# Optimization experiments

Measured on AMD Instinct MI355X. Metric: run time of the kernel, lower is better.

## Reference

```python
import jax, jax.numpy as jnp
import numpy as np

B, S, H, NH, DK, VOCAB, FF, L = 512, 64, 512, 8, 64, 2000, 2048, 6


def _pos_enc():
    pos = jnp.arange(S, dtype=jnp.float32)[:, None]           # [S,1]
    i = jnp.arange(H // 2, dtype=jnp.float32)                  # [H/2]
    ang = pos / (10000.0 ** (2.0 * i / H))                     # [S,H/2]
    pe = jnp.zeros((S, H), jnp.float32)
    pe = pe.at[:, 0::2].set(jnp.sin(ang)).at[:, 1::2].set(jnp.cos(ang))
    return pe


def _ln(x, g, b, eps=1e-5):
    m = x.mean(-1, keepdims=True)
    v = ((x - m) ** 2).mean(-1, keepdims=True)
    return (x - m) / jnp.sqrt(v + eps) * g + b


def _heads(x, w):  # x:[B,S,H] w:[H,H] -> [B,NH,S,DK]
    return (x @ w.T).reshape(B, S, NH, DK).transpose(0, 2, 1, 3)


def _sdpa(Q, K, V, keep):  # keep: bool mask broadcastable to [B,NH,S,S]
    scores = jnp.einsum('bhqd,bhkd->bhqk', Q, K) / np.sqrt(DK).astype(np.float32)
    scores = jnp.where(keep, scores, -1e9)
    return jnp.einsum('bhqk,bhkd->bhqd', jax.nn.softmax(scores, axis=-1), V)


def _merge(z, wo):  # [B,NH,S,DK] -> [B,S,H] -> out proj
    return z.transpose(0, 2, 1, 3).reshape(B, S, H) @ wo.T


def setup_inputs():
    key = jax.random.key(0)
    ks = jax.random.split(key, 30)
    n = lambda k, sh: jax.random.normal(k, sh, jnp.float32) * 0.02
    inp = {
        'source_ids': jax.random.randint(ks[0], (B, S), 0, VOCAB),
        'target_ids': jax.random.randint(ks[1], (B, S), 0, VOCAB),
        'source_mask': jnp.ones((B, S), jnp.int32),
        'target_mask': jnp.ones((B, S), jnp.int32),
        'src_emb': n(ks[2], (VOCAB, H)),
        'tgt_emb': n(ks[3], (VOCAB, H)),
        'enc_wq': n(ks[4], (L, H, H)), 'enc_wk': n(ks[5], (L, H, H)),
        'enc_wv': n(ks[6], (L, H, H)), 'enc_wo': n(ks[7], (L, H, H)),
        'enc_ln_g': jnp.ones((L, H), jnp.float32), 'enc_ln_b': jnp.zeros((L, H), jnp.float32),
        'enc_fc1_w': n(ks[8], (L, FF, H)), 'enc_fc1_b': jnp.zeros((L, FF), jnp.float32),
        'enc_fc2_w': n(ks[9], (L, H, FF)), 'enc_fc2_b': jnp.zeros((L, H), jnp.float32),
        'dec_mwq': n(ks[10], (L, H, H)), 'dec_mwk': n(ks[11], (L, H, H)),
        'dec_mwv': n(ks[12], (L, H, H)), 'dec_mwo': n(ks[13], (L, H, H)),
        'dec_cwq': n(ks[14], (L, H, H)), 'dec_cwo': n(ks[15], (L, H, H)),
        'dec_ln_g': jnp.ones((L, H), jnp.float32), 'dec_ln_b': jnp.zeros((L, H), jnp.float32),
        'dec_fc_w': n(ks[16], (L, H, H)), 'dec_fc_b': jnp.zeros((L, H), jnp.float32),
    }
    return inp


def reference(source_ids, target_ids, source_mask, target_mask, src_emb, tgt_emb,
              enc_wq, enc_wk, enc_wv, enc_wo, enc_ln_g, enc_ln_b,
              enc_fc1_w, enc_fc1_b, enc_fc2_w, enc_fc2_b,
              dec_mwq, dec_mwk, dec_mwv, dec_mwo, dec_cwq, dec_cwo,
              dec_ln_g, dec_ln_b, dec_fc_w, dec_fc_b):
    pe = _pos_enc()
    x = src_emb[source_ids] + pe              # [B,S,H]
    y = tgt_emb[target_ids] + pe
    src_keep = (source_mask != 0)[:, None, None, :]                 # [B,1,1,S]
    causal = jnp.tril(jnp.ones((S, S), bool))
    tgt_keep = (target_mask != 0)[:, None, None, :] & causal[None, None]  # [B,1,S,S]

    Kenc = Venc = None
    for l in range(L):
        Q, K, Vh = _heads(x, enc_wq[l]), _heads(x, enc_wk[l]), _heads(x, enc_wv[l])
        z = _merge(_sdpa(Q, K, Vh, src_keep), enc_wo[l])
        x = _ln(x + z, enc_ln_g[l], enc_ln_b[l])
        f = (x @ enc_fc1_w[l].T + enc_fc1_b[l]) @ enc_fc2_w[l].T + enc_fc2_b[l]
        x = _ln(x + f, enc_ln_g[l], enc_ln_b[l])
        Kenc, Venc = K, Vh  # last encoder block's K,V feed decoder cross-attn

    for l in range(L):
        Q, K, Vh = _heads(y, dec_mwq[l]), _heads(y, dec_mwk[l]), _heads(y, dec_mwv[l])
        z1 = _merge(_sdpa(Q, K, Vh, tgt_keep), dec_mwo[l])
        t1 = _ln(y + z1, dec_ln_g[l], dec_ln_b[l])
        Qc = _heads(t1, dec_cwq[l])
        # NOTE: original applies the TARGET mask to encoder keys (faithful)
        z2 = _merge(_sdpa(Qc, Kenc, Venc, tgt_keep), dec_cwo[l])
        t2 = _ln(t1 + z2, dec_ln_g[l], dec_ln_b[l])
        t3 = t2 @ dec_fc_w[l].T + dec_fc_b[l]
        y = _ln(t2 + t3, dec_ln_g[l], dec_ln_b[l])
    return y
```

## Files before the change

kernel.cpp:

```cpp
#include <hip/hip_runtime.h>

typedef unsigned short u16;
typedef u16 u16x8 __attribute__((ext_vector_type(8)));
typedef __bf16 bf16x8 __attribute__((ext_vector_type(8)));
typedef float f32x4 __attribute__((ext_vector_type(4)));

#define TTOK 32768
#define HD 512
#define FFD 2048
#define SLEN 64
#define EW 262144

__device__ __forceinline__ float b2f(u16 u) {
  union { float f; unsigned int i; } v; v.i = ((unsigned int)u) << 16; return v.f;
}
__device__ __forceinline__ u16 f2b(float f) {
  union { float f; unsigned int i; } v; v.f = f;
  unsigned int i = v.i;
  return (u16)((i + 0x7FFFu + ((i >> 16) & 1u)) >> 16);
}

__device__ __forceinline__ void gload16(const u16* g, u16* l) {
  __builtin_amdgcn_global_load_lds((const __attribute__((address_space(1))) void*)g,
                                   (__attribute__((address_space(3))) void*)l,
                                   16, 0, 0);
}

__device__ __forceinline__ f32x4 mfma16(bf16x8 a, bf16x8 b, f32x4 c) {
  return __builtin_amdgcn_mfma_f32_16x16x32_bf16(a, b, c, 0, 0, 0);
}

__global__ __launch_bounds__(256) void pe_kernel(float* __restrict__ pe) {
  int idx = blockIdx.x * 256 + threadIdx.x;
  int s = idx >> 9, h = idx & 511;
  float e2i = (float)(h & ~1);
  float ang = (float)s * powf(10000.0f, -e2i * (1.0f / 512.0f));
  pe[idx] = (h & 1) ? cosf(ang) : sinf(ang);
}

struct WArgs {
  const float* src[13];
  unsigned long long dstoff[13];
  unsigned npl[13];
  unsigned dstride[13];
  unsigned cum[14];
};

__global__ __launch_bounds__(256) void wconv_all(WArgs a, u16* __restrict__ Wb) {
  unsigned i = ((unsigned)blockIdx.x * 256 + threadIdx.x) * 8;
  int t = 0;
  #pragma unroll
  for (int k = 1; k < 13; ++k) if (i >= a.cum[k]) t = k;
  unsigned local = i - a.cum[t];
  unsigned l = local / a.npl[t];
  unsigned r = local - l * a.npl[t];
  const float* s = a.src[t] + local;
  f32x4 x0 = *(const f32x4*)s, x1 = *(const f32x4*)(s + 4);
  u16x8 o;
  #pragma unroll
  for (int k = 0; k < 4; ++k) { o[k] = f2b(x0[k]); o[4 + k] = f2b(x1[k]); }
  *(u16x8*)(Wb + a.dstoff[t] + (size_t)l * a.dstride[t] + r) = o;
}

__global__ __launch_bounds__(256) void embed_kernel(
    const int* __restrict__ ids, const float* __restrict__ emb,
    const float* __restrict__ pe, u16* __restrict__ outB) {
  int chunk = blockIdx.x * 256 + threadIdx.x;
  int t = chunk >> 6;
  int c8 = (chunk & 63) * 8;
  int s = t & (SLEN - 1);
  int id = ids[t];
  const float* e = emb + (size_t)id * HD + c8;
  const float* p = pe + s * HD + c8;
  f32x4 e0 = *(const f32x4*)e, e1 = *(const f32x4*)(e + 4);
  f32x4 p0 = *(const f32x4*)p, p1 = *(const f32x4*)(p + 4);
  u16x8 ob;
  #pragma unroll
  for (int i = 0; i < 4; ++i) {
    ob[i]     = f2b(e0[i] + p0[i]);
    ob[4 + i] = f2b(e1[i] + p1[i]);
  }
  *(u16x8*)(outB + (size_t)t * HD + c8) = ob;
}

template<int F32OUT>
__global__ __launch_bounds__(256) void ln_kernel(
    const u16* A, const u16* __restrict__ Z, int ldz,
    const float* __restrict__ g, const float* __restrict__ b,
    u16* outB, float* outF) {
  int row = blockIdx.x * 4 + (threadIdx.x >> 6);
  int lane = threadIdx.x & 63;
  size_t base = (size_t)row * HD + lane * 8;
  size_t zbase = (size_t)row * ldz + lane * 8;
  u16x8 av = *(const u16x8*)(A + base);
  u16x8 zv = *(const u16x8*)(Z + zbase);
  float x[8];
  float s = 0.f;
  #pragma unroll
  for (int i = 0; i < 8; ++i) { x[i] = b2f(av[i]) + b2f(zv[i]); s += x[i]; }
  #pragma unroll
  for (int off = 32; off; off >>= 1) s += __shfl_xor(s, off);
  float m = s * (1.0f / HD);
  float vs = 0.f;
  #pragma unroll
  for (int i = 0; i < 8; ++i) { float d = x[i] - m; vs += d * d; }
  #pragma unroll
  for (int off = 32; off; off >>= 1) vs += __shfl_xor(vs, off);
  float rstd = rsqrtf(vs * (1.0f / HD) + 1e-5f);
  f32x4 g0 = *(const f32x4*)(g + lane * 8), g1 = *(const f32x4*)(g + lane * 8 + 4);
  f32x4 b0 = *(const f32x4*)(b + lane * 8), b1 = *(const f32x4*)(b + lane * 8 + 4);
  float o[8];
  #pragma unroll
  for (int i = 0; i < 4; ++i) {
    o[i]     = (x[i] - m) * rstd * g0[i] + b0[i];
    o[4 + i] = (x[4 + i] - m) * rstd * g1[i] + b1[i];
  }
  if (F32OUT) {
    f32x4 o0, o1;
    #pragma unroll
    for (int i = 0; i < 4; ++i) { o0[i] = o[i]; o1[i] = o[4 + i]; }
    *(f32x4*)(outF + base) = o0;
    *(f32x4*)(outF + base + 4) = o1;
  } else {
    u16x8 ob;
    #pragma unroll
    for (int i = 0; i < 8; ++i) ob[i] = f2b(o[i]);
    *(u16x8*)(outB + base) = ob;
  }
}

#define BAR() __builtin_amdgcn_s_barrier()
#define WAIT_LGKM0() asm volatile("s_waitcnt lgkmcnt(0)" ::: "memory")
#define WAIT_VM8()   asm volatile("s_waitcnt vmcnt(8)" ::: "memory")
#define WAIT_VM5()   asm volatile("s_waitcnt vmcnt(5)" ::: "memory")
#define WAIT_VM3()   asm volatile("s_waitcnt vmcnt(3)" ::: "memory")
#define WAIT_VM0()   asm volatile("s_waitcnt vmcnt(0)" ::: "memory")

template<int BIAS>
__global__ __launch_bounds__(512, 4) void gemm128(
    const u16* __restrict__ A, const u16* __restrict__ Bw,
    const float* __restrict__ bias, u16* __restrict__ Cb,
    int nbn, int K, int lda, int ldb, int ldc) {
  __shared__ u16 lds[24576];
  const int tid = threadIdx.x;
  const int lane = tid & 63, w = tid >> 6;
  const int wr = w >> 2, wc = w & 3;
  const int l15 = lane & 15, lq = lane >> 4;

  const int cpx = gridDim.x >> 3;
  const int L = (blockIdx.x & 7) * cpx + (blockIdx.x >> 3);
  const int bm = (L / nbn) * 128, bn = (L % nbn) * 256;

  const u16 *pa, *pb0, *pb1;
  {
    int p = tid * 16;
    int row = p >> 6;
    int lb = ((((p >> 4) & 3) ^ ((row >> 2) & 3)) << 4) | (p & 15);
    pa = A + (size_t)(bm + row) * lda + (lb >> 1);
    int r0 = p >> 6;
    int lb0 = ((((p >> 4) & 3) ^ ((r0 >> 2) & 3)) << 4) | (p & 15);
    pb0 = Bw + (size_t)(bn + r0) * ldb + (lb0 >> 1);
    int p1 = p + 8192;
    int r1 = p1 >> 6;
    int lb1 = ((((p1 >> 4) & 3) ^ ((r1 >> 2) & 3)) << 4) | (p1 & 15);
    pb1 = Bw + (size_t)(bn + r1) * ldb + (lb1 >> 1);
  }

  int offA[4], offB[4];
  #pragma unroll
  for (int mf = 0; mf < 4; ++mf) {
    int row = wr * 64 + mf * 16 + l15;
    offA[mf] = row * 32 + ((lq ^ ((row >> 2) & 3)) << 3);
  }
  #pragma unroll
  for (int j = 0; j < 4; ++j) {
    int row = wc * 64 + j * 16 + l15;
    offB[j] = row * 32 + ((lq ^ ((row >> 2) & 3)) << 3);
  }

  const int NS = K >> 5;

#define STAGE(s, sl) { \
    gload16(pa  + (s) * 32, &lds[(sl) * 4096 + w * 512]); \
    gload16(pb0 + (s) * 32, &lds[8192 + (sl) * 8192 + w * 512]); \
    gload16(pb1 + (s) * 32, &lds[8192 + (sl) * 8192 + w * 512 + 4096]); }

  f32x4 acc[4][4] = {};

  STAGE(0, 0);
  for (int h = 0; h < NS; ++h) {
    int nh = h + 1; if (nh > NS - 1) nh = NS - 1;
    STAGE(nh, (h + 1) & 1);
    WAIT_VM3();
    BAR();
    const int sa = (h & 1) * 4096, sb = 8192 + (h & 1) * 8192;
    bf16x8 af[4], bf4[4];
    #pragma unroll
    for (int i = 0; i < 4; ++i) af[i] = *(const bf16x8*)&lds[sa + offA[i]];
    #pragma unroll
    for (int j = 0; j < 4; ++j) bf4[j] = *(const bf16x8*)&lds[sb + offB[j]];
    WAIT_LGKM0();
    __builtin_amdgcn_s_setprio(1);
    #pragma unroll
    for (int mf = 0; mf < 4; ++mf)
      #pragma unroll
      for (int j = 0; j < 4; ++j)
        acc[mf][j] = mfma16(af[mf], bf4[j], acc[mf][j]);
    __builtin_amdgcn_s_setprio(0);
    BAR();
  }
  WAIT_VM0();

  #pragma unroll
  for (int q = 0; q < 4; ++q) {
    BAR();
    if (wr == (q >> 1)) {
      #pragma unroll
      for (int mi = 0; mi < 2; ++mi) {
        int mf = (q & 1) * 2 + mi;
        #pragma unroll
        for (int j = 0; j < 4; ++j)
          #pragma unroll
          for (int r = 0; r < 4; ++r) {
            int lrow = mi * 16 + lq * 4 + r;
            int col = wc * 64 + j * 16 + l15;
            int byt = (lrow * 1024 + col * 4) ^ (((lrow >> 2) & 3) << 6);
            *(float*)((char*)lds + byt) = acc[mf][j][r];
          }
      }
    }
    WAIT_LGKM0();
    BAR();
    #pragma unroll
    for (int k = 0; k < 2; ++k) {
      int c = tid + k * 512;
      int row = c >> 5, c32 = c & 31;
      int byt = (row * 1024 + c32 * 32) ^ (((row >> 2) & 3) << 6);
      f32x4 v0 = *(const f32x4*)((const char*)lds + byt);
      f32x4 v1 = *(const f32x4*)((const char*)lds + byt + 16);
      int gcol = bn + c32 * 8;
      size_t off = (size_t)(bm + q * 32 + row) * ldc + gcol;
      if (BIAS) {
        f32x4 bb0 = *(const f32x4*)(bias + gcol);
        f32x4 bb1 = *(const f32x4*)(bias + gcol + 4);
        #pragma unroll
        for (int i = 0; i < 4; ++i) { v0[i] += bb0[i]; v1[i] += bb1[i]; }
      }
      u16x8 ob;
      #pragma unroll
      for (int i = 0; i < 4; ++i) { ob[i] = f2b(v0[i]); ob[4 + i] = f2b(v1[i]); }
      *(u16x8*)(Cb + off) = ob;
    }
  }
#undef STAGE
}

template<int BIAS, int ACC>
__global__ __launch_bounds__(512, 2) void gemm256(
    const u16* __restrict__ A, const u16* __restrict__ Bw,
    const float* __restrict__ bias, u16* __restrict__ Cb,
    int nbn, int K, int lda, int ldb, int ldc) {
  __shared__ u16 lds[65536];
  const int tid = threadIdx.x;
  const int lane = tid & 63, w = tid >> 6;
  const int wr = w >> 2, wc = w & 3;
  const int l15 = lane & 15, lq = lane >> 4;

  const int cpx = gridDim.x >> 3;
  const int L = (blockIdx.x & 7) * cpx + (blockIdx.x >> 3);
  const int bm = (L / nbn) * 256, bn = (L % nbn) * 256;

  const u16 *pa0, *pa1, *pb0, *pb1;
  {
    int p0 = w * 1024 + lane * 16;
    int p1 = p0 + 8192;
    int lb0 = p0 ^ (((p0 >> 7) & 7) << 4);
    int lb1 = p1 ^ (((p1 >> 7) & 7) << 4);
    int r0 = (lb0 >> 7) + (((lb0 >> 6) & 1) << 7);
    int r1 = (lb1 >> 7) + (((lb1 >> 6) & 1) << 7);
    int c0 = (lb0 & 63) >> 1;
    int c1 = (lb1 & 63) >> 1;
    pa0 = A  + (size_t)(bm + r0) * lda + c0;
    pa1 = A  + (size_t)(bm + r1) * lda + c1;
    pb0 = Bw + (size_t)(bn + r0) * ldb + c0;
    pb1 = Bw + (size_t)(bn + r1) * ldb + c1;
  }
  const int dst = w * 512;

  int offA[8], offB[4];
  #pragma unroll
  for (int mf = 0; mf < 8; ++mf) {
    int rowp = mf * 16 + l15;
    offA[mf] = ((rowp * 128 + wr * 64 + lq * 16) ^ ((l15 & 7) << 4)) >> 1;
  }
  #pragma unroll
  for (int j = 0; j < 4; ++j) {
    int rB = wc * 64 + j * 16 + l15;
    int rowp = rB & 127, cg = rB >> 7;
    offB[j] = ((rowp * 128 + cg * 64 + lq * 16) ^ ((l15 & 7) << 4)) >> 1;
  }

  const int NK2 = K >> 5;
  const int NT  = K >> 6;

#define STAGEA(kh, slot) { \
    gload16(pa0 + (kh) * 32, &lds[(slot) * 8192 + dst]); \
    gload16(pa1 + (kh) * 32, &lds[(slot) * 8192 + dst + 4096]); }
#define STAGEB(kh, slot) { \
    gload16(pb0 + (kh) * 32, &lds[32768 + (slot) * 8192 + dst]); \
    gload16(pb1 + (kh) * 32, &lds[32768 + (slot) * 8192 + dst + 4096]); }
#define LDA4(slot, mh) { \
    _Pragma("unroll") for (int i = 0; i < 4; ++i) \
      af[i] = *(const bf16x8*)&lds[(slot) * 8192 + offA[(mh) * 4 + i]]; }
#define LDB4(slot) { \
    _Pragma("unroll") for (int j = 0; j < 4; ++j) \
      bf[j] = *(const bf16x8*)&lds[32768 + (slot) * 8192 + offB[j]]; }
#define MFMA16(mh) { \
    __builtin_amdgcn_s_setprio(1); \
    _Pragma("unroll") for (int i = 0; i < 4; ++i) \
      _Pragma("unroll") for (int j = 0; j < 4; ++j) \
        acc[(mh) * 4 + i][j] = mfma16(af[i], bf[j], acc[(mh) * 4 + i][j]); \
    __builtin_amdgcn_s_setprio(0); }

  f32x4 acc[8][4] = {};
  bf16x8 af[4], bf[4];

  STAGEA(0, 0); STAGEB(0, 0);
  STAGEA(1, 1); STAGEB(1, 1);
  STAGEA(2, 2); STAGEB(2, 2);
  WAIT_VM8();
  BAR();

  for (int t = 0; t < NT; ++t) {
    const int s0 = (2 * t) & 3, s1 = (2 * t + 1) & 3;
    int kh3 = 2 * t + 3; if (kh3 > NK2 - 1) kh3 = NK2 - 1;
    int kh4 = 2 * t + 4; if (kh4 > NK2 - 1) kh4 = NK2 - 1;
    const int w3 = (2 * t + 3) & 3, w4 = (2 * t + 4) & 3;

    LDB4(s0); LDA4(s0, 0);
    STAGEA(kh3, w3);
    BAR(); WAIT_LGKM0();
    MFMA16(0);
    BAR();

    LDA4(s0, 1);
    STAGEB(kh3, w3);
    BAR(); WAIT_LGKM0();
    MFMA16(1);
    WAIT_VM8();
    BAR();

    LDB4(s1); LDA4(s1, 0);
    STAGEA(kh4, w4);
    BAR(); WAIT_LGKM0();
    MFMA16(0);
    BAR();

    LDA4(s1, 1);
    STAGEB(kh4, w4);
    BAR(); WAIT_LGKM0();
    MFMA16(1);
    WAIT_VM8();
    BAR();
  }
  WAIT_VM0();

  #pragma unroll
  for (int h = 0; h < 2; ++h) {
    BAR();
    if (wr == h) {
      #pragma unroll
      for (int mf = 0; mf < 8; ++mf)
        #pragma unroll
        for (int j = 0; j < 4; ++j)
          #pragma unroll
          for (int r = 0; r < 4; ++r) {
            int row = mf * 16 + lq * 4 + r;
            int col = wc * 64 + j * 16 + l15;
            int byt = (row * 1024 + col * 4) ^ (((row >> 2) & 1) << 6);
            *(float*)((char*)lds + byt) = acc[mf][j][r];
          }
    }
    WAIT_LGKM0();
    BAR();
    #pragma unroll
    for (int k = 0; k < 8; ++k) {
      int c = tid + k * 512;
      int row = c >> 5, c32 = c & 31;
      int byt = (row * 1024 + c32 * 32) ^ (((row >> 2) & 1) << 6);
      f32x4 v0 = *(const f32x4*)((const char*)lds + byt);
      f32x4 v1 = *(const f32x4*)((const char*)lds + byt + 16);
      int gcol = bn + c32 * 8;
      size_t off = (size_t)(bm + h * 128 + row) * ldc + gcol;
      if (BIAS) {
        f32x4 bb0 = *(const f32x4*)(bias + gcol);
        f32x4 bb1 = *(const f32x4*)(bias + gcol + 4);
        #pragma unroll
        for (int i = 0; i < 4; ++i) { v0[i] += bb0[i]; v1[i] += bb1[i]; }
      }
      u16x8 ob;
      if (ACC) {
        u16x8 cr = *(const u16x8*)(Cb + off);
        #pragma unroll
        for (int i = 0; i < 4; ++i) {
          ob[i]     = f2b(v0[i] + b2f(cr[i]));
          ob[4 + i] = f2b(v1[i] + b2f(cr[4 + i]));
        }
      } else {
        #pragma unroll
        for (int i = 0; i < 4; ++i) { ob[i] = f2b(v0[i]); ob[4 + i] = f2b(v1[i]); }
      }
      *(u16x8*)(Cb + off) = ob;
    }
  }
#undef STAGEA
#undef STAGEB
#undef LDA4
#undef LDB4
#undef MFMA16
}

template<int BIAS, int F32OUT>
__global__ __launch_bounds__(512, 2) void gemm_ln(
    const u16* __restrict__ A, const u16* __restrict__ Bw,
    const float* __restrict__ bias,
    const u16* __restrict__ resid, const float* __restrict__ g,
    const float* __restrict__ bv,
    u16* outB, float* outF, int K, int lda, int ldb) {
  __shared__ u16 lds[40960];
  const int tid = threadIdx.x;
  const int lane = tid & 63, w = tid >> 6;
  const int l15 = lane & 15, lq = lane >> 4;

  const int cpx = gridDim.x >> 3;
  const int L = (blockIdx.x & 7) * cpx + (blockIdx.x >> 3);
  const int bm = L * 128;

  const u16* pa;
  const u16* pb[4];
  {
    int p = tid * 16;
    int row = p >> 6;
    int lb = ((((p >> 4) & 3) ^ ((row >> 2) & 3)) << 4) | (p & 15);
    pa = A + (size_t)(bm + row) * lda + (lb >> 1);
    #pragma unroll
    for (int c = 0; c < 4; ++c) {
      int q = c * 8192 + tid * 16;
      int rowb = q >> 6;
      int lbb = ((((q >> 4) & 3) ^ ((rowb >> 2) & 3)) << 4) | (q & 15);
      pb[c] = Bw + (size_t)rowb * ldb + (lbb >> 1);
    }
  }

  int offA[8], offB[4];
  #pragma unroll
  for (int mf = 0; mf < 8; ++mf) {
    int row = mf * 16 + l15;
    offA[mf] = row * 32 + ((lq ^ ((row >> 2) & 3)) << 3);
  }
  #pragma unroll
  for (int j = 0; j < 4; ++j) {
    int row = w * 64 + j * 16 + l15;
    offB[j] = row * 32 + ((lq ^ ((row >> 2) & 3)) << 3);
  }

  const int NS = K >> 5;

#define STAGE(s, sl) { \
    gload16(pa + (s) * 32, &lds[(sl) * 4096 + w * 512]); \
    _Pragma("unroll") for (int c = 0; c < 4; ++c) \
      gload16(pb[c] + (s) * 32, &lds[8192 + (sl) * 16384 + c * 4096 + w * 512]); }

  f32x4 acc[8][4] = {};

  STAGE(0, 0);
  for (int h = 0; h < NS; ++h) {
    int nh = h + 1; if (nh > NS - 1) nh = NS - 1;
    STAGE(nh, (h + 1) & 1);
    WAIT_VM5();
    BAR();
    const int sa = (h & 1) * 4096, sb = 8192 + (h & 1) * 16384;
    bf16x8 af[8], bf4[4];
    #pragma unroll
    for (int i = 0; i < 8; ++i) af[i] = *(const bf16x8*)&lds[sa + offA[i]];
    #pragma unroll
    for (int j = 0; j < 4; ++j) bf4[j] = *(const bf16x8*)&lds[sb + offB[j]];
    WAIT_LGKM0();
    __builtin_amdgcn_s_setprio(1);
    #pragma unroll
    for (int mf = 0; mf < 8; ++mf)
      #pragma unroll
      for (int j = 0; j < 4; ++j)
        acc[mf][j] = mfma16(af[mf], bf4[j], acc[mf][j]);
    __builtin_amdgcn_s_setprio(0);
    BAR();
  }
  WAIT_VM0();

  float bias4[4] = {0.f, 0.f, 0.f, 0.f};
  if (BIAS) {
    #pragma unroll
    for (int j = 0; j < 4; ++j) bias4[j] = bias[w * 64 + j * 16 + l15];
  }
  const f32x4 gv0 = *(const f32x4*)(g + lane * 8);
  const f32x4 gv1 = *(const f32x4*)(g + lane * 8 + 4);
  const f32x4 bv0 = *(const f32x4*)(bv + lane * 8);
  const f32x4 bv1 = *(const f32x4*)(bv + lane * 8 + 4);

  #pragma unroll
  for (int q = 0; q < 4; ++q) {
    BAR();
    #pragma unroll
    for (int mi = 0; mi < 2; ++mi) {
      int mf = 2 * q + mi;
      #pragma unroll
      for (int j = 0; j < 4; ++j)
        #pragma unroll
        for (int r = 0; r < 4; ++r) {
          int lrow = mi * 16 + lq * 4 + r;
          int col = w * 64 + j * 16 + l15;
          int byt = (lrow * 2048 + col * 4) ^ (((lrow >> 2) & 3) << 6);
          *(float*)((char*)lds + byt) = acc[mf][j][r] + bias4[j];
        }
    }
    WAIT_LGKM0();
    BAR();
    #pragma unroll
    for (int rr = 0; rr < 4; ++rr) {
      int lrow = w * 4 + rr;
      int grow = bm + q * 32 + lrow;
      int byt = (lrow * 2048 + lane * 32) ^ (((lrow >> 2) & 3) << 6);
      f32x4 z0 = *(const f32x4*)((const char*)lds + byt);
      f32x4 z1 = *(const f32x4*)((const char*)lds + byt + 16);
      u16x8 av = *(const u16x8*)(resid + (size_t)grow * HD + lane * 8);
      float x[8];
      float s = 0.f;
      #pragma unroll
      for (int i = 0; i < 4; ++i) {
        x[i] = b2f(av[i]) + z0[i];
        x[4 + i] = b2f(av[4 + i]) + z1[i];
      }
      #pragma unroll
      for (int i = 0; i < 8; ++i) s += x[i];
      #pragma unroll
      for (int off = 32; off; off >>= 1) s += __shfl_xor(s, off);
      float m = s * (1.0f / HD);
      float vs = 0.f;
      #pragma unroll
      for (int i = 0; i < 8; ++i) { float d = x[i] - m; vs += d * d; }
      #pragma unroll
      for (int off = 32; off; off >>= 1) vs += __shfl_xor(vs, off);
      float rstd = rsqrtf(vs * (1.0f / HD) + 1e-5f);
      float o[8];
      #pragma unroll
      for (int i = 0; i < 4; ++i) {
        o[i]     = (x[i] - m) * rstd * gv0[i] + bv0[i];
        o[4 + i] = (x[4 + i] - m) * rstd * gv1[i] + bv1[i];
      }
      if (F32OUT) {
        f32x4 o0, o1;
        #pragma unroll
        for (int i = 0; i < 4; ++i) { o0[i] = o[i]; o1[i] = o[4 + i]; }
        *(f32x4*)(outF + (size_t)grow * HD + lane * 8) = o0;
        *(f32x4*)(outF + (size_t)grow * HD + lane * 8 + 4) = o1;
      } else {
        u16x8 ob;
        #pragma unroll
        for (int i = 0; i < 8; ++i) ob[i] = f2b(o[i]);
        *(u16x8*)(outB + (size_t)grow * HD + lane * 8) = ob;
      }
    }
  }
#undef STAGE
}

template<int CAUSAL, int SAVEKV>
__global__ __launch_bounds__(256) void attn_kernel(
    u16* Q, const u16* __restrict__ Kb, const u16* __restrict__ Vb,
    const int* __restrict__ mask, int qld, int kvld, u16* __restrict__ kvdst) {
  __shared__ u16 Ks[64 * 72];
  __shared__ u16 Vt[64 * 72];
  __shared__ u16 Ps[4][16 * 72];
  const int bh = blockIdx.x;
  const int b = bh >> 3, h = bh & 7;
  const int h0 = h * 64;
  const int tid = threadIdx.x, lane = tid & 63, w = tid >> 6;
  const size_t qbase = (size_t)b * 64 * qld + h0;
  const size_t kbase = (size_t)b * 64 * kvld + h0;
  const int l15 = lane & 15, l16 = (lane >> 4) * 8;

  {
    int r = tid >> 2;
    int c = (tid & 3) * 16;
    const u16* ksrc = Kb + kbase + (size_t)r * kvld + c;
    u16x8 k0 = *(const u16x8*)ksrc;
    u16x8 k1 = *(const u16x8*)(ksrc + 8);
    *(u16x8*)&Ks[r * 72 + c]     = k0;
    *(u16x8*)&Ks[r * 72 + c + 8] = k1;
    const u16* vsrc = Vb + kbase + (size_t)r * kvld + c;
    u16x8 t0 = *(const u16x8*)vsrc;
    u16x8 t1 = *(const u16x8*)(vsrc + 8);
    #pragma unroll
    for (int i = 0; i < 8; ++i) {
      Vt[(c + i) * 72 + r]     = t0[i];
      Vt[(c + 8 + i) * 72 + r] = t1[i];
    }
    if (SAVEKV) {
      size_t db = (size_t)(b * 64 + r) * 1024 + h0 + c;
      *(u16x8*)(kvdst + db)       = k0;
      *(u16x8*)(kvdst + db + 8)   = k1;
      *(u16x8*)(kvdst + db + 512) = t0;
      *(u16x8*)(kvdst + db + 520) = t1;
    }
  }
  const int qrow = w * 16 + l15;
  const u16* qp = Q + qbase + (size_t)qrow * qld;
  bf16x8 qf0 = *(const bf16x8*)&qp[l16];
  bf16x8 qf1 = *(const bf16x8*)&qp[32 + l16];
  __syncthreads();

  f32x4 sc[4] = {};
  #pragma unroll
  for (int nf = 0; nf < 4; ++nf) {
    bf16x8 k0 = *(const bf16x8*)&Ks[(nf * 16 + l15) * 72 + l16];
    bf16x8 k1 = *(const bf16x8*)&Ks[(nf * 16 + l15) * 72 + 32 + l16];
    sc[nf] = mfma16(qf0, k0, sc[nf]);
    sc[nf] = mfma16(qf1, k1, sc[nf]);
  }
  int mk[4];
  #pragma unroll
  for (int nf = 0; nf < 4; ++nf) mk[nf] = mask[b * 64 + nf * 16 + l15];
  float pv[4][4];
  #pragma unroll
  for (int r = 0; r < 4; ++r) {
    int q = w * 16 + (lane >> 4) * 4 + r;
    #pragma unroll
    for (int nf = 0; nf < 4; ++nf) {
      int k = nf * 16 + l15;
      bool kp = (mk[nf] != 0);
      if (CAUSAL) kp = kp && (k <= q);
      pv[r][nf] = kp ? sc[nf][r] * 0.125f : -1e9f;
    }
  }
  #pragma unroll
  for (int r = 0; r < 4; ++r) {
    float mx = fmaxf(fmaxf(pv[r][0], pv[r][1]), fmaxf(pv[r][2], pv[r][3]));
    #pragma unroll
    for (int off = 1; off < 16; off <<= 1) mx = fmaxf(mx, __shfl_xor(mx, off));
    float sum = 0.f;
    #pragma unroll
    for (int nf = 0; nf < 4; ++nf) { pv[r][nf] = __expf(pv[r][nf] - mx); sum += pv[r][nf]; }
    #pragma unroll
    for (int off = 1; off < 16; off <<= 1) sum += __shfl_xor(sum, off);
    float inv = 1.0f / sum;
    #pragma unroll
    for (int nf = 0; nf < 4; ++nf) pv[r][nf] *= inv;
  }
  #pragma unroll
  for (int r = 0; r < 4; ++r) {
    int q = (lane >> 4) * 4 + r;
    #pragma unroll
    for (int nf = 0; nf < 4; ++nf)
      Ps[w][q * 72 + nf * 16 + l15] = f2b(pv[r][nf]);
  }
  f32x4 oacc[4] = {};
  #pragma unroll
  for (int kk = 0; kk < 2; ++kk) {
    bf16x8 pa = *(const bf16x8*)&Ps[w][l15 * 72 + kk * 32 + l16];
    #pragma unroll
    for (int df = 0; df < 4; ++df) {
      bf16x8 vf = *(const bf16x8*)&Vt[(df * 16 + l15) * 72 + kk * 32 + l16];
      oacc[df] = mfma16(pa, vf, oacc[df]);
    }
  }
  #pragma unroll
  for (int df = 0; df < 4; ++df) {
    int col = df * 16 + l15;
    #pragma unroll
    for (int r = 0; r < 4; ++r) {
      int t = w * 16 + (lane >> 4) * 4 + r;
      Q[qbase + (size_t)t * qld + col] = f2b(oacc[df][r]);
    }
  }
}

extern "C" void kernel_launch(void* const* d_in, const int* in_sizes, int n_in,
                              void* d_out, int out_size, void* d_ws, size_t ws_size,
                              hipStream_t stream) {
  const int* src_ids    = (const int*)d_in[0];
  const int* tgt_ids    = (const int*)d_in[1];
  const int* src_mask   = (const int*)d_in[2];
  const int* tgt_mask   = (const int*)d_in[3];
  const float* src_emb  = (const float*)d_in[4];
  const float* tgt_emb  = (const float*)d_in[5];
  const float* enc_wq = (const float*)d_in[6];
  const float* enc_wk = (const float*)d_in[7];
  const float* enc_wv = (const float*)d_in[8];
  const float* enc_wo = (const float*)d_in[9];
  const float* enc_g  = (const float*)d_in[10];
  const float* enc_b  = (const float*)d_in[11];
  const float* fc1w = (const float*)d_in[12];
  const float* fc1b = (const float*)d_in[13];
  const float* fc2w = (const float*)d_in[14];
  const float* fc2b = (const float*)d_in[15];
  const float* mwq = (const float*)d_in[16];
  const float* mwk = (const float*)d_in[17];
  const float* mwv = (const float*)d_in[18];
  const float* mwo = (const float*)d_in[19];
  const float* cwq = (const float*)d_in[20];
  const float* cwo = (const float*)d_in[21];
  const float* dec_g = (const float*)d_in[22];
  const float* dec_b = (const float*)d_in[23];
  const float* dfw = (const float*)d_in[24];
  const float* dfb = (const float*)d_in[25];
  float* outF = (float*)d_out;
  u16* kvenc = (u16*)d_out;

  constexpr size_t SZ_PE  = (size_t)SLEN * HD * 4;
  constexpr size_t SZ_W   = (size_t)114 * EW * 2;
  constexpr size_t SZ_CUR = (size_t)TTOK * HD * 2;
  constexpr size_t SZ_QKV = (size_t)TTOK * 1536 * 2;
  constexpr size_t SZ_R   = (size_t)TTOK * FFD * 2;
  constexpr size_t SZ_Z2  = (size_t)TTOK * HD * 2;
  constexpr size_t NEED_SMALL = SZ_PE + SZ_W + SZ_CUR + SZ_QKV;
  constexpr size_t NEED_BIG   = SZ_PE + SZ_W + SZ_CUR + SZ_R + SZ_Z2;
  if (ws_size < NEED_SMALL) return;
  const bool big = (ws_size >= NEED_BIG);

  char* ws = (char*)d_ws;
  float* pe = (float*)ws;
  u16* W    = (u16*)(ws + SZ_PE);
  u16* cur  = (u16*)(ws + SZ_PE + SZ_W);
  u16* qkv  = (u16*)(ws + SZ_PE + SZ_W + SZ_CUR);
  u16* z2   = big ? (u16*)(ws + SZ_PE + SZ_W + SZ_CUR + SZ_R)
                  : qkv + (size_t)TTOK * 1024;

  dim3 blk(256), blk5(512);
  const unsigned int E = EW, S_E = 12 * EW, S_D = 7 * EW;
  u16* WD = W + (size_t)72 * EW;

  pe_kernel<<<128, blk, 0, stream>>>(pe);

  {
    WArgs wa;
    const float* srcs[13] = {enc_wq, enc_wk, enc_wv, enc_wo, fc1w, fc2w,
                             mwq, mwk, mwv, mwo, cwq, cwo, dfw};
    const unsigned long long dstoffs[13] = {
        0ull, (unsigned long long)E, 2ull * E, 3ull * E, 4ull * E, 8ull * E,
        72ull * E, 73ull * E, 74ull * E, 75ull * E, 76ull * E, 77ull * E, 78ull * E};
    const unsigned npls[13] = {E, E, E, E, 4 * E, 4 * E, E, E, E, E, E, E, E};
    const unsigned cumsE[14] = {0, 6, 12, 18, 24, 48, 72, 78, 84, 90, 96, 102, 108, 114};
    for (int t = 0; t < 13; ++t) {
      wa.src[t] = srcs[t];
      wa.dstoff[t] = dstoffs[t];
      wa.npl[t] = npls[t];
      wa.dstride[t] = (t < 6) ? S_E : S_D;
    }
    for (int t = 0; t < 14; ++t) wa.cum[t] = cumsE[t] * E;
    wconv_all<<<14592, blk, 0, stream>>>(wa, W);
  }

  embed_kernel<<<8192, blk, 0, stream>>>(src_ids, src_emb, pe, cur);
  for (int l = 0; l < 6; ++l) {
    const u16* Wl = W + (size_t)l * S_E;
    const float* g  = enc_g + (size_t)l * HD;
    const float* bb = enc_b + (size_t)l * HD;
    const float* b1 = fc1b + (size_t)l * FFD;
    const float* b2 = fc2b + (size_t)l * HD;

    gemm128<0><<<1536, blk5, 0, stream>>>(cur, Wl, nullptr, qkv, 6, 512, 512, 512, 1536);
    if (l == 5)
      attn_kernel<0,1><<<4096, blk, 0, stream>>>(qkv, qkv + 512, qkv + 1024, src_mask, 1536, 1536, kvenc);
    else
      attn_kernel<0,0><<<4096, blk, 0, stream>>>(qkv, qkv + 512, qkv + 1024, src_mask, 1536, 1536, nullptr);
    if (big) {
      gemm_ln<0,0><<<256, blk5, 0, stream>>>(qkv, Wl + 3 * E, nullptr, cur, g, bb, cur, nullptr, 512, 1536, 512);
      gemm128<1><<<2048, blk5, 0, stream>>>(cur, Wl + 4 * E, b1, qkv, 8, 512, 512, 512, 2048);
      gemm_ln<1,0><<<256, blk5, 0, stream>>>(qkv, Wl + 8 * E, b2, cur, g, bb, cur, nullptr, 2048, 2048, 2048);
    } else {
      gemm256<0,0><<<256, blk5, 0, stream>>>(qkv, Wl + 3 * E, nullptr, qkv + 1024, 2, 512, 1536, 512, 1536);
      ln_kernel<0><<<8192, blk, 0, stream>>>(cur, qkv + 1024, 1536, g, bb, cur, nullptr);
      gemm256<1,0><<<512, blk5, 0, stream>>>(cur, Wl + 4 * E, b1,        qkv, 4, 512, 512, 512, 1024);
      gemm256<1,0><<<256, blk5, 0, stream>>>(qkv, Wl + 8 * E, b2,        z2,  2, 1024, 1024, 2048, 512);
      gemm256<1,0><<<512, blk5, 0, stream>>>(cur, Wl + 6 * E, b1 + 1024, qkv, 4, 512, 512, 512, 1024);
      gemm256<0,1><<<256, blk5, 0, stream>>>(qkv, Wl + 8 * E + 1024, nullptr, z2, 2, 1024, 1024, 2048, 512);
      ln_kernel<0><<<8192, blk, 0, stream>>>(cur, z2, 512, g, bb, cur, nullptr);
    }
  }

  embed_kernel<<<8192, blk, 0, stream>>>(tgt_ids, tgt_emb, pe, cur);
  for (int l = 0; l < 6; ++l) {
    const u16* Wl = WD + (size_t)l * S_D;
    const float* g  = dec_g + (size_t)l * HD;
    const float* bb = dec_b + (size_t)l * HD;
    const float* fb = dfb + (size_t)l * HD;

    gemm128<0><<<1536, blk5, 0, stream>>>(cur, Wl, nullptr, qkv, 6, 512, 512, 512, 1536);
    attn_kernel<1,0><<<4096, blk, 0, stream>>>(qkv, qkv + 512, qkv + 1024, tgt_mask, 1536, 1536, nullptr);
    if (big) {
      gemm_ln<0,0><<<256, blk5, 0, stream>>>(qkv, Wl + 3 * E, nullptr, cur, g, bb, cur, nullptr, 512, 1536, 512);
      gemm128<0><<<512, blk5, 0, stream>>>(cur, Wl + 4 * E, nullptr, qkv, 2, 512, 512, 512, 1536);
      attn_kernel<1,0><<<4096, blk, 0, stream>>>(qkv, kvenc, kvenc + 512, tgt_mask, 1536, 1024, nullptr);
      gemm_ln<0,0><<<256, blk5, 0, stream>>>(qkv, Wl + 5 * E, nullptr, cur, g, bb, cur, nullptr, 512, 1536, 512);
      if (l == 5)
        gemm_ln<1,1><<<256, blk5, 0, stream>>>(cur, Wl + 6 * E, fb, cur, g, bb, nullptr, outF, 512, 512, 512);
      else
        gemm_ln<1,0><<<256, blk5, 0, stream>>>(cur, Wl + 6 * E, fb, cur, g, bb, cur, nullptr, 512, 512, 512);
    } else {
      gemm256<0,0><<<256, blk5, 0, stream>>>(qkv, Wl + 3 * E, nullptr, qkv + 1024, 2, 512, 1536, 512, 1536);
      ln_kernel<0><<<8192, blk, 0, stream>>>(cur, qkv + 1024, 1536, g, bb, cur, nullptr);
      gemm256<0,0><<<256, blk5, 0, stream>>>(cur, Wl + 4 * E, nullptr, qkv, 2, 512, 512, 512, 1536);
      attn_kernel<1,0><<<4096, blk, 0, stream>>>(qkv, kvenc, kvenc + 512, tgt_mask, 1536, 1024, nullptr);
      gemm256<0,0><<<256, blk5, 0, stream>>>(qkv, Wl + 5 * E, nullptr, qkv + 1024, 2, 512, 1536, 512, 1536);
      ln_kernel<0><<<8192, blk, 0, stream>>>(cur, qkv + 1024, 1536, g, bb, cur, nullptr);
      gemm256<1,0><<<256, blk5, 0, stream>>>(cur, Wl + 6 * E, fb, qkv, 2, 512, 512, 512, 512);
      if (l == 5)
        ln_kernel<1><<<8192, blk, 0, stream>>>(cur, qkv, 512, g, bb, nullptr, outF);
      else
        ln_kernel<0><<<8192, blk, 0, stream>>>(cur, qkv, 512, g, bb, cur, nullptr);
    }
  }
  (void)in_sizes; (void)n_in; (void)out_size;
}
```

Measured before the change: 3.339 ms.

## Run fused GEMM+LayerNorm with 16 waves in a 2x8 warp grid

The fused GEMM-LayerNorm kernel is rebuilt to use 1024 threads (16 waves) per 128x512 tile instead of 512. Waves are arranged as 2 row groups by 8 column groups, so each wave holds a 64x64 accumulator instead of 128x64. Only the first 8 waves load A, the vmcnt waits are adjusted per wave, and the LN epilogue writes its staging through the row-group owner. This halves per-wave register pressure and doubles the waves available to hide latency, at the cost of more barrier participants and some idle loaders.

```diff
diff --git a/kernel.cpp b/kernel.cpp
--- a/kernel.cpp
+++ b/kernel.cpp
@@ -132,8 +132,8 @@
 #define BAR() __builtin_amdgcn_s_barrier()
 #define WAIT_LGKM0() asm volatile("s_waitcnt lgkmcnt(0)" ::: "memory")
 #define WAIT_VM8()   asm volatile("s_waitcnt vmcnt(8)" ::: "memory")
-#define WAIT_VM5()   asm volatile("s_waitcnt vmcnt(5)" ::: "memory")
 #define WAIT_VM3()   asm volatile("s_waitcnt vmcnt(3)" ::: "memory")
+#define WAIT_VM2()   asm volatile("s_waitcnt vmcnt(2)" ::: "memory")
 #define WAIT_VM0()   asm volatile("s_waitcnt vmcnt(0)" ::: "memory")
 
 template<int BIAS>
@@ -421,7 +421,7 @@
 }
 
 template<int BIAS, int F32OUT>
-__global__ __launch_bounds__(512, 2) void gemm_ln(
+__global__ __launch_bounds__(1024, 4) void gemm_ln16(
     const u16* __restrict__ A, const u16* __restrict__ Bw,
     const float* __restrict__ bias,
     const u16* __restrict__ resid, const float* __restrict__ g,
@@ -430,65 +430,66 @@
   __shared__ u16 lds[40960];
   const int tid = threadIdx.x;
   const int lane = tid & 63, w = tid >> 6;
+  const int wr = w >> 3, wc = w & 7;
   const int l15 = lane & 15, lq = lane >> 4;
 
   const int cpx = gridDim.x >> 3;
   const int L = (blockIdx.x & 7) * cpx + (blockIdx.x >> 3);
   const int bm = L * 128;
 
-  const u16* pa;
-  const u16* pb[4];
+  const u16 *pa, *pb0, *pb1;
   {
-    int p = tid * 16;
+    int p = (tid * 16) & 8191;
     int row = p >> 6;
     int lb = ((((p >> 4) & 3) ^ ((row >> 2) & 3)) << 4) | (p & 15);
     pa = A + (size_t)(bm + row) * lda + (lb >> 1);
-    #pragma unroll
-    for (int c = 0; c < 4; ++c) {
-      int q = c * 8192 + tid * 16;
-      int rowb = q >> 6;
-      int lbb = ((((q >> 4) & 3) ^ ((rowb >> 2) & 3)) << 4) | (q & 15);
-      pb[c] = Bw + (size_t)rowb * ldb + (lbb >> 1);
-    }
-  }
-
-  int offA[8], offB[4];
-  #pragma unroll
-  for (int mf = 0; mf < 8; ++mf) {
-    int row = mf * 16 + l15;
+    int q0 = tid * 16;
+    int r0 = q0 >> 6;
+    int lb0 = ((((q0 >> 4) & 3) ^ ((r0 >> 2) & 3)) << 4) | (q0 & 15);
+    pb0 = Bw + (size_t)r0 * ldb + (lb0 >> 1);
+    int q1 = q0 + 16384;
+    int r1 = q1 >> 6;
+    int lb1 = ((((q1 >> 4) & 3) ^ ((r1 >> 2) & 3)) << 4) | (q1 & 15);
+    pb1 = Bw + (size_t)r1 * ldb + (lb1 >> 1);
+  }
+
+  int offA[4], offB[4];
+  #pragma unroll
+  for (int mf = 0; mf < 4; ++mf) {
+    int row = wr * 64 + mf * 16 + l15;
     offA[mf] = row * 32 + ((lq ^ ((row >> 2) & 3)) << 3);
   }
   #pragma unroll
   for (int j = 0; j < 4; ++j) {
-    int row = w * 64 + j * 16 + l15;
+    int row = wc * 64 + j * 16 + l15;
     offB[j] = row * 32 + ((lq ^ ((row >> 2) & 3)) << 3);
   }
 
   const int NS = K >> 5;
 
 #define STAGE(s, sl) { \
-    gload16(pa + (s) * 32, &lds[(sl) * 4096 + w * 512]); \
-    _Pragma("unroll") for (int c = 0; c < 4; ++c) \
-      gload16(pb[c] + (s) * 32, &lds[8192 + (sl) * 16384 + c * 4096 + w * 512]); }
-
-  f32x4 acc[8][4] = {};
+    if (w < 8) gload16(pa + (s) * 32, &lds[(sl) * 4096 + w * 512]); \
+    gload16(pb0 + (s) * 32, &lds[8192 + (sl) * 16384 + w * 512]); \
+    gload16(pb1 + (s) * 32, &lds[8192 + (sl) * 16384 + 8192 + w * 512]); }
+
+  f32x4 acc[4][4] = {};
 
   STAGE(0, 0);
   for (int h = 0; h < NS; ++h) {
     int nh = h + 1; if (nh > NS - 1) nh = NS - 1;
     STAGE(nh, (h + 1) & 1);
-    WAIT_VM5();
+    if (w < 8) { WAIT_VM3(); } else { WAIT_VM2(); }
     BAR();
     const int sa = (h & 1) * 4096, sb = 8192 + (h & 1) * 16384;
-    bf16x8 af[8], bf4[4];
-    #pragma unroll
-    for (int i = 0; i < 8; ++i) af[i] = *(const bf16x8*)&lds[sa + offA[i]];
+    bf16x8 af[4], bf4[4];
+    #pragma unroll
+    for (int i = 0; i < 4; ++i) af[i] = *(const bf16x8*)&lds[sa + offA[i]];
     #pragma unroll
     for (int j = 0; j < 4; ++j) bf4[j] = *(const bf16x8*)&lds[sb + offB[j]];
     WAIT_LGKM0();
     __builtin_amdgcn_s_setprio(1);
     #pragma unroll
-    for (int mf = 0; mf < 8; ++mf)
+    for (int mf = 0; mf < 4; ++mf)
       #pragma unroll
       for (int j = 0; j < 4; ++j)
         acc[mf][j] = mfma16(af[mf], bf4[j], acc[mf][j]);
@@ -500,7 +501,7 @@
   float bias4[4] = {0.f, 0.f, 0.f, 0.f};
   if (BIAS) {
     #pragma unroll
-    for (int j = 0; j < 4; ++j) bias4[j] = bias[w * 64 + j * 16 + l15];
+    for (int j = 0; j < 4; ++j) bias4[j] = bias[wc * 64 + j * 16 + l15];
   }
   const f32x4 gv0 = *(const f32x4*)(g + lane * 8);
   const f32x4 gv1 = *(const f32x4*)(g + lane * 8 + 4);
@@ -510,24 +511,26 @@
   #pragma unroll
   for (int q = 0; q < 4; ++q) {
     BAR();
-    #pragma unroll
-    for (int mi = 0; mi < 2; ++mi) {
-      int mf = 2 * q + mi;
-      #pragma unroll
-      for (int j = 0; j < 4; ++j)
+    if (wr == (q >> 1)) {
+      #pragma unroll
+      for (int mi = 0; mi < 2; ++mi) {
+        int mf = (q & 1) * 2 + mi;
         #pragma unroll
-        for (int r = 0; r < 4; ++r) {
-          int lrow = mi * 16 + lq * 4 + r;
-          int col = w * 64 + j * 16 + l15;
-          int byt = (lrow * 2048 + col * 4) ^ (((lrow >> 2) & 3) << 6);
-          *(float*)((char*)lds + byt) = acc[mf][j][r] + bias4[j];
-        }
+        for (int j = 0; j < 4; ++j)
+          #pragma unroll
+          for (int r = 0; r < 4; ++r) {
+            int lrow = mi * 16 + lq * 4 + r;
+            int col = wc * 64 + j * 16 + l15;
+            int byt = (lrow * 2048 + col * 4) ^ (((lrow >> 2) & 3) << 6);
+            *(float*)((char*)lds + byt) = acc[mf][j][r] + bias4[j];
+          }
+      }
     }
     WAIT_LGKM0();
     BAR();
     #pragma unroll
-    for (int rr = 0; rr < 4; ++rr) {
-      int lrow = w * 4 + rr;
+    for (int rr = 0; rr < 2; ++rr) {
+      int lrow = w * 2 + rr;
       int grow = bm + q * 32 + lrow;
       int byt = (lrow * 2048 + lane * 32) ^ (((lrow >> 2) & 3) << 6);
       f32x4 z0 = *(const f32x4*)((const char*)lds + byt);
@@ -735,7 +738,7 @@
   u16* z2   = big ? (u16*)(ws + SZ_PE + SZ_W + SZ_CUR + SZ_R)
                   : qkv + (size_t)TTOK * 1024;
 
-  dim3 blk(256), blk5(512);
+  dim3 blk(256), blk5(512), blkX(1024);
   const unsigned int E = EW, S_E = 12 * EW, S_D = 7 * EW;
   u16* WD = W + (size_t)72 * EW;
 
@@ -774,9 +777,9 @@
     else
       attn_kernel<0,0><<<4096, blk, 0, stream>>>(qkv, qkv + 512, qkv + 1024, src_mask, 1536, 1536, nullptr);
     if (big) {
-      gemm_ln<0,0><<<256, blk5, 0, stream>>>(qkv, Wl + 3 * E, nullptr, cur, g, bb, cur, nullptr, 512, 1536, 512);
+      gemm_ln16<0,0><<<256, blkX, 0, stream>>>(qkv, Wl + 3 * E, nullptr, cur, g, bb, cur, nullptr, 512, 1536, 512);
       gemm128<1><<<2048, blk5, 0, stream>>>(cur, Wl + 4 * E, b1, qkv, 8, 512, 512, 512, 2048);
-      gemm_ln<1,0><<<256, blk5, 0, stream>>>(qkv, Wl + 8 * E, b2, cur, g, bb, cur, nullptr, 2048, 2048, 2048);
+      gemm_ln16<1,0><<<256, blkX, 0, stream>>>(qkv, Wl + 8 * E, b2, cur, g, bb, cur, nullptr, 2048, 2048, 2048);
     } else {
       gemm256<0,0><<<256, blk5, 0, stream>>>(qkv, Wl + 3 * E, nullptr, qkv + 1024, 2, 512, 1536, 512, 1536);
       ln_kernel<0><<<8192, blk, 0, stream>>>(cur, qkv + 1024, 1536, g, bb, cur, nullptr);
@@ -798,14 +801,14 @@
     gemm128<0><<<1536, blk5, 0, stream>>>(cur, Wl, nullptr, qkv, 6, 512, 512, 512, 1536);
     attn_kernel<1,0><<<4096, blk, 0, stream>>>(qkv, qkv + 512, qkv + 1024, tgt_mask, 1536, 1536, nullptr);
     if (big) {
-      gemm_ln<0,0><<<256, blk5, 0, stream>>>(qkv, Wl + 3 * E, nullptr, cur, g, bb, cur, nullptr, 512, 1536, 512);
+      gemm_ln16<0,0><<<256, blkX, 0, stream>>>(qkv, Wl + 3 * E, nullptr, cur, g, bb, cur, nullptr, 512, 1536, 512);
       gemm128<0><<<512, blk5, 0, stream>>>(cur, Wl + 4 * E, nullptr, qkv, 2, 512, 512, 512, 1536);
       attn_kernel<1,0><<<4096, blk, 0, stream>>>(qkv, kvenc, kvenc + 512, tgt_mask, 1536, 1024, nullptr);
-      gemm_ln<0,0><<<256, blk5, 0, stream>>>(qkv, Wl + 5 * E, nullptr, cur, g, bb, cur, nullptr, 512, 1536, 512);
+      gemm_ln16<0,0><<<256, blkX, 0, stream>>>(qkv, Wl + 5 * E, nullptr, cur, g, bb, cur, nullptr, 512, 1536, 512);
       if (l == 5)
-        gemm_ln<1,1><<<256, blk5, 0, stream>>>(cur, Wl + 6 * E, fb, cur, g, bb, nullptr, outF, 512, 512, 512);
+        gemm_ln16<1,1><<<256, blkX, 0, stream>>>(cur, Wl + 6 * E, fb, cur, g, bb, nullptr, outF, 512, 512, 512);
       else
-        gemm_ln<1,0><<<256, blk5, 0, stream>>>(cur, Wl + 6 * E, fb, cur, g, bb, cur, nullptr, 512, 512, 512);
+        gemm_ln16<1,0><<<256, blkX, 0, stream>>>(cur, Wl + 6 * E, fb, cur, g, bb, cur, nullptr, 512, 512, 512);
     } else {
       gemm256<0,0><<<256, blk5, 0, stream>>>(qkv, Wl + 3 * E, nullptr, qkv + 1024, 2, 512, 1536, 512, 1536);
       ln_kernel<0><<<8192, blk, 0, stream>>>(cur, qkv + 1024, 1536, g, bb, cur, nullptr);
```

After: 3.723 ms. +11.5%, slower.
